# Kernel tuning notes

Measured on AMD Instinct MI355X. Metric: run time of the kernel, lower is better.

## Reference

```python
import jax, jax.numpy as jnp
import numpy as np

GROUP = 64   # quantization group size (nunchaku W4A4 default)
QMAX = 7.0   # symmetric int4 positive range


def setup_inputs() -> dict:
    key = jax.random.key(0)
    ks = jax.random.split(key, 6)
    T, K, N, R = 256, 3072, 3072, 32
    x = jax.random.normal(ks[0], (T, K), dtype=jnp.float32)
    # int4 weight codes stored as 0..15 (dequant subtracts zero-point 8)
    qweight = jax.random.randint(ks[1], (N, K), 0, 16, dtype=jnp.int32)
    # per-(out_channel, input_group) weight scales, small positive
    wscales = jax.random.uniform(ks[2], (N, K // GROUP), dtype=jnp.float32) * 0.02 + 1e-3
    lora_down = jax.random.normal(ks[3], (R, K), dtype=jnp.float32) / np.sqrt(K)
    lora_up = jax.random.normal(ks[4], (N, R), dtype=jnp.float32) / np.sqrt(R)
    bias = jax.random.normal(ks[5], (N,), dtype=jnp.float32) * 0.01
    return {"x": x, "qweight": qweight, "wscales": wscales,
            "lora_down": lora_down, "lora_up": lora_up, "bias": bias}


def _quantize_act(x):
    # per-token, per-group symmetric int4 fake-quant (quantize -> dequantize)
    T, K = x.shape
    xg = x.reshape(T, K // GROUP, GROUP)
    scale = jnp.maximum(jnp.max(jnp.abs(xg), axis=-1, keepdims=True) / QMAX, 1e-8)
    q = jnp.clip(jnp.round(xg / scale), -8.0, QMAX)
    return (q * scale).reshape(T, K)


def reference(x, qweight, wscales, lora_down, lora_up, bias):
    # Dequantize int4 weights: (code - 8) * per-group scale  -> [N, K]
    N, K = qweight.shape
    w = (qweight.astype(jnp.float32) - 8.0).reshape(N, K // GROUP, GROUP)
    w = (w * wscales[:, :, None]).reshape(N, K)
    # W4A4 main path: int4-quantized activations x dequantized int4 weights
    x_dq = _quantize_act(x)
    main = x_dq @ w.T                               # [T, N]
    # fused low-rank (SVDQuant LoRA) branch on full-precision activations
    lora = (x @ lora_down.T) @ lora_up.T            # [T, R] @ [R, N]
    return main + lora + bias
```

## Files before the change

kernel.cpp:

```cpp
#include <hip/hip_runtime.h>
#include <stdint.h>

#define T_DIM 256
#define K_DIM 3072
#define N_DIM 3072
#define R_DIM 32
#define KG    48
#define NSPLIT 6

#define PQ_BLOCKS 4608
#define QA_BLOCKS 3072
#define LM_BLOCKS 96

typedef __bf16 bf16x8 __attribute__((ext_vector_type(8)));
typedef float  f32x4  __attribute__((ext_vector_type(4)));
typedef unsigned short u16x8 __attribute__((ext_vector_type(8)));

__device__ __forceinline__ unsigned short f2bf(float f) {
    unsigned u = __builtin_bit_cast(unsigned, f);
    unsigned rounding = 0x7FFFu + ((u >> 16) & 1u);
    return (unsigned short)((u + rounding) >> 16);
}

__device__ __forceinline__ bf16x8 cvt8(const float* p) {
    float4 lo = ((const float4*)p)[0], hi = ((const float4*)p)[1];
    bf16x8 v;
    v[0] = (__bf16)lo.x; v[1] = (__bf16)lo.y; v[2] = (__bf16)lo.z; v[3] = (__bf16)lo.w;
    v[4] = (__bf16)hi.x; v[5] = (__bf16)hi.y; v[6] = (__bf16)hi.z; v[7] = (__bf16)hi.w;
    return v;
}

__global__ __launch_bounds__(256) void prep(
        const int*   __restrict__ qweight,
        const float* __restrict__ x,
        const float* __restrict__ lora_down,
        unsigned*       __restrict__ Qp,
        unsigned short* __restrict__ Ap,
        float*          __restrict__ Lm) {
    int blk = blockIdx.x;
    if (blk < PQ_BLOCKS) {
        size_t o = (size_t)blk * 256 + threadIdx.x;
        unsigned kt  = (unsigned)(o / 24576u);
        unsigned rem = (unsigned)(o % 24576u);
        unsigned n = rem >> 3, wi = rem & 7;
        const int4* p = (const int4*)(qweight + (size_t)n * K_DIM + (size_t)kt * 64 + wi * 8);
        int4 a = p[0], b = p[1];
        unsigned w = (unsigned)(a.x & 15)        | ((unsigned)(a.y & 15) << 4)
                   | ((unsigned)(a.z & 15) << 8) | ((unsigned)(a.w & 15) << 12)
                   | ((unsigned)(b.x & 15) << 16)| ((unsigned)(b.y & 15) << 20)
                   | ((unsigned)(b.z & 15) << 24)| ((unsigned)(b.w & 15) << 28);
        Qp[o] = w;
    } else if (blk < PQ_BLOCKS + QA_BLOCKS) {
        int widx = (blk - PQ_BLOCKS) * 4 + (threadIdx.x >> 6);
        int lane = threadIdx.x & 63;
        int t = widx / KG, g = widx % KG;
        float v = x[(size_t)t * K_DIM + g * 64 + lane];
        float a = fabsf(v);
        #pragma unroll
        for (int off = 32; off; off >>= 1) a = fmaxf(a, __shfl_xor(a, off));
        float scale = fmaxf(a / 7.0f, 1e-8f);
        float q = rintf(v / scale);
        q = fminf(fmaxf(q, -8.f), 7.f);
        Ap[(((size_t)g * 8 + (lane >> 3)) * 256 + t) * 8 + (lane & 7)] = f2bf(q * scale);
    } else {
        int kb = blk - PQ_BLOCKS - QA_BLOCKS;
        int lane = threadIdx.x & 63, wv = threadIdx.x >> 6;
        int mrow = lane & 15, quad = lane >> 4;
        int k0 = kb * 32 + quad * 8;
        bf16x8 a[4], b[2];
        #pragma unroll
        for (int mt = 0; mt < 4; ++mt)
            a[mt] = cvt8(x + (size_t)(wv * 64 + mt * 16 + mrow) * K_DIM + k0);
        #pragma unroll
        for (int nt = 0; nt < 2; ++nt)
            b[nt] = cvt8(lora_down + (size_t)(nt * 16 + mrow) * K_DIM + k0);
        f32x4 acc[4][2];
        f32x4 zero = {0.f, 0.f, 0.f, 0.f};
        #pragma unroll
        for (int i = 0; i < 4; ++i) { acc[i][0] = zero; acc[i][1] = zero; }
        #pragma unroll
        for (int mt = 0; mt < 4; ++mt)
            #pragma unroll
            for (int nt = 0; nt < 2; ++nt)
                acc[mt][nt] = __builtin_amdgcn_mfma_f32_16x16x32_bf16(
                    a[mt], b[nt], acc[mt][nt], 0, 0, 0);
        #pragma unroll
        for (int mt = 0; mt < 4; ++mt)
            #pragma unroll
            for (int nt = 0; nt < 2; ++nt)
                #pragma unroll
                for (int r = 0; r < 4; ++r)
                    atomicAdd(&Lm[(size_t)(wv * 64 + mt * 16 + quad * 4 + r) * R_DIM
                                  + nt * 16 + mrow], acc[mt][nt][r]);
    }
}

__global__ __launch_bounds__(256) void gemm_main(
        const uint4*    __restrict__ ApU,
        const unsigned* __restrict__ Qp,
        const float*    __restrict__ wscales,
        const float*    __restrict__ Lm,
        const float*    __restrict__ lora_up,
        float*          __restrict__ P) {
    __shared__ uint4 BsU[2][512];
    int nblk  = blockIdx.x;
    int mblk  = blockIdx.y;
    int split = blockIdx.z;
    int c0 = split * (KG / NSPLIT);
    int c1 = (split == NSPLIT - 1) ? KG + 1 : c0 + (KG / NSPLIT);
    int tid = threadIdx.x;
    int lane = tid & 63, wv = tid >> 6;
    int mrow = lane & 15, quad = lane >> 4;
    int n_row = tid >> 2, seg = tid & 3;
    const int nbase = nblk * 64;
    const int mbase = mblk * 128 + wv * 32;

    f32x4 acc[2][4];
    f32x4 zero = {0.f, 0.f, 0.f, 0.f};
    #pragma unroll
    for (int i = 0; i < 2; ++i)
        #pragma unroll
        for (int j = 0; j < 4; ++j) acc[i][j] = zero;

    uint2 ubc[2];
    float wsr[2];
    bf16x8 af[2][2][2];

    const float* wsrow = wscales + (size_t)(nbase + n_row) * KG;

    #define AFRAG(kt, ks, mt) \
        (*(const bf16x8*)&ApU[(size_t)(kt) * 2048 + ((ks) * 4 + quad) * 256 + \
                              mbase + (mt) * 16 + mrow])

    {
        #pragma unroll
        for (int ks = 0; ks < 2; ++ks)
            #pragma unroll
            for (int mt = 0; mt < 2; ++mt)
                af[0][ks][mt] = AFRAG(c0, ks, mt);
        const unsigned* q0 = Qp + ((size_t)c0 * N_DIM + nbase + n_row) * 8 + seg * 2;
        const unsigned* q1 = Qp + ((size_t)(c0 + 1) * N_DIM + nbase + n_row) * 8 + seg * 2;
        ubc[0] = *(const uint2*)q0;
        ubc[1] = *(const uint2*)q1;
        wsr[0] = wsrow[c0];
        wsr[1] = wsrow[c0 + 1];
    }

    #define STEP(PP, KT)                                                          \
    {                                                                             \
        constexpr int p = (PP);                                                   \
        const int kk = (KT);                                                      \
        if (kk < KG) {                                                            \
            float w = wsr[p];                                                     \
            float m8w = -8.0f * w;                                                \
            unsigned u0 = ubc[p].x, u1 = ubc[p].y;                                \
            unsigned e0 = u0 & 0x0F0F0F0Fu, od0 = (u0 >> 4) & 0x0F0F0F0Fu;        \
            unsigned e1 = u1 & 0x0F0F0F0Fu, od1 = (u1 >> 4) & 0x0F0F0F0Fu;        \
            bf16x8 v0, v1;                                                        \
            _Pragma("unroll")                                                     \
            for (int j = 0; j < 4; ++j) {                                         \
                v0[2*j]   = (__bf16)__builtin_fmaf((float)((e0  >> (8*j)) & 0xFFu), w, m8w); \
                v0[2*j+1] = (__bf16)__builtin_fmaf((float)((od0 >> (8*j)) & 0xFFu), w, m8w); \
                v1[2*j]   = (__bf16)__builtin_fmaf((float)((e1  >> (8*j)) & 0xFFu), w, m8w); \
                v1[2*j+1] = (__bf16)__builtin_fmaf((float)((od1 >> (8*j)) & 0xFFu), w, m8w); \
            }                                                                     \
            BsU[p][(seg * 2 + 0) * 64 + n_row] = __builtin_bit_cast(uint4, v0);   \
            BsU[p][(seg * 2 + 1) * 64 + n_row] = __builtin_bit_cast(uint4, v1);   \
        } else {                                                                  \
            bf16x8 v0 = __builtin_bit_cast(bf16x8, (u16x8)(0));                   \
            bf16x8 v1 = __builtin_bit_cast(bf16x8, (u16x8)(0));                   \
            if (seg < 2) {                                                        \
                const float* lu = lora_up + (size_t)(nbase + n_row) * R_DIM + seg * 16; \
                _Pragma("unroll")                                                 \
                for (int j = 0; j < 8; ++j) {                                     \
                    v0[j] = (__bf16)lu[j];                                        \
                    v1[j] = (__bf16)lu[8 + j];                                    \
                }                                                                 \
            }                                                                     \
            BsU[p][(seg * 2 + 0) * 64 + n_row] = __builtin_bit_cast(uint4, v0);   \
            BsU[p][(seg * 2 + 1) * 64 + n_row] = __builtin_bit_cast(uint4, v1);   \
        }                                                                         \
        __syncthreads();                                                          \
        if (kk + 2 < c1 && kk + 2 < KG) {                                         \
            const unsigned* q2 = Qp + ((size_t)(kk + 2) * N_DIM + nbase + n_row) * 8 + seg * 2; \
            ubc[p] = *(const uint2*)q2;                                           \
            wsr[p] = wsrow[kk + 2];                                               \
        }                                                                         \
        if (kk + 1 < c1) {                                                        \
            if (kk + 1 < KG) {                                                    \
                _Pragma("unroll")                                                 \
                for (int ks = 0; ks < 2; ++ks)                                    \
                    _Pragma("unroll")                                             \
                    for (int mt = 0; mt < 2; ++mt)                                \
                        af[p ^ 1][ks][mt] = AFRAG(kk + 1, ks, mt);                \
            } else {                                                              \
                _Pragma("unroll")                                                 \
                for (int mt = 0; mt < 2; ++mt) {                                  \
                    int row = mbase + mt * 16 + mrow;                             \
                    if (quad < 4)                                                 \
                        af[p ^ 1][0][mt] = cvt8(Lm + (size_t)row * R_DIM + quad * 8); \
                    else                                                          \
                        af[p ^ 1][0][mt] = __builtin_bit_cast(bf16x8, (u16x8)(0)); \
                    af[p ^ 1][1][mt] = __builtin_bit_cast(bf16x8, (u16x8)(0));    \
                }                                                                 \
            }                                                                     \
        }                                                                         \
        _Pragma("unroll")                                                         \
        for (int ks = 0; ks < 2; ++ks) {                                          \
            bf16x8 b[4];                                                          \
            _Pragma("unroll")                                                     \
            for (int nt = 0; nt < 4; ++nt)                                        \
                b[nt] = *(const bf16x8*)&BsU[p][(ks * 4 + quad) * 64 + nt * 16 + mrow]; \
            _Pragma("unroll")                                                     \
            for (int mt = 0; mt < 2; ++mt)                                        \
                _Pragma("unroll")                                                 \
                for (int nt = 0; nt < 4; ++nt)                                    \
                    acc[mt][nt] = __builtin_amdgcn_mfma_f32_16x16x32_bf16(        \
                        af[p][ks][mt], b[nt], acc[mt][nt], 0, 0, 0);              \
        }                                                                         \
    }

    int kt = c0;
    for (; kt + 1 < c1; kt += 2) {
        STEP(0, kt);
        STEP(1, kt + 1);
    }
    if (kt < c1) STEP(0, kt);

    #undef STEP
    #undef AFRAG
    float* Pp = P + (size_t)split * (T_DIM * N_DIM);
    #pragma unroll
    for (int nt = 0; nt < 4; ++nt) {
        int n = nbase + nt * 16 + mrow;
        #pragma unroll
        for (int mt = 0; mt < 2; ++mt) {
            int row0 = mblk * 128 + wv * 32 + mt * 16 + quad * 4;
            #pragma unroll
            for (int r = 0; r < 4; ++r)
                Pp[(size_t)(row0 + r) * N_DIM + n] = acc[mt][nt][r];
        }
    }
}

__global__ __launch_bounds__(256) void reduce_out(
        const float4* __restrict__ P, const float* __restrict__ bias,
        float4* __restrict__ out) {
    int i = blockIdx.x * 256 + threadIdx.x;
    const int STRIDE = T_DIM * N_DIM / 4;
    float4 bv = *(const float4*)&bias[(i * 4) % N_DIM];
    float4 o = bv;
    #pragma unroll
    for (int s = 0; s < NSPLIT; ++s) {
        float4 v = P[i + s * STRIDE];
        o.x += v.x; o.y += v.y; o.z += v.z; o.w += v.w;
    }
    out[i] = o;
}

extern "C" void kernel_launch(void* const* d_in, const int* in_sizes, int n_in,
                              void* d_out, int out_size, void* d_ws, size_t ws_size,
                              hipStream_t stream) {
    const float* x         = (const float*)d_in[0];
    const int*   qweight   = (const int*)d_in[1];
    const float* wscales   = (const float*)d_in[2];
    const float* lora_down = (const float*)d_in[3];
    const float* lora_up   = (const float*)d_in[4];
    const float* bias      = (const float*)d_in[5];

    char* wsp = (char*)d_ws;
    unsigned short* Ap = (unsigned short*)wsp;
    wsp += (size_t)KG * 2048 * 16;
    float* Lm = (float*)wsp;
    wsp += (size_t)T_DIM * R_DIM * 4;
    unsigned* Qp = (unsigned*)wsp;
    wsp += (size_t)N_DIM * (K_DIM / 8) * 4;
    float* P = (float*)wsp;

    hipMemsetAsync(Lm, 0, (size_t)T_DIM * R_DIM * sizeof(float), stream);
    prep<<<PQ_BLOCKS + QA_BLOCKS + LM_BLOCKS, 256, 0, stream>>>(
        qweight, x, lora_down, Qp, Ap, Lm);
    gemm_main<<<dim3(48, 2, NSPLIT), 256, 0, stream>>>(
        (const uint4*)Ap, Qp, wscales, Lm, lora_up, P);
    reduce_out<<<(T_DIM * N_DIM / 4) / 256, 256, 0, stream>>>(
        (const float4*)P, bias, (float4*)d_out);
}
```

Before: 117.4 us.

## Replace split-K partial buffer and reduce kernel with atomic accumulation into output

The prep kernel gains extra blocks that initialise the output with the broadcast bias. The GEMM then atomically adds each split-K partial tile straight into the output, so the per-split partial buffer and the separate reduce kernel go away. This removes one launch and the write and re-read of six full-size partial matrices. In exchange it adds global float atomics with six-way contention per element and makes the summation order nondeterministic. The LDS fragment load is also rewritten as a uint4 read plus bit_cast.

Measured after the change: 119.3 us. Within noise of the previous version (+1.6%).

```diff
diff --git a/kernel.cpp b/kernel.cpp
--- a/kernel.cpp
+++ b/kernel.cpp
@@ -11,6 +11,7 @@
 #define PQ_BLOCKS 4608
 #define QA_BLOCKS 3072
 #define LM_BLOCKS 96
+#define BO_BLOCKS 768
 
 typedef __bf16 bf16x8 __attribute__((ext_vector_type(8)));
 typedef float  f32x4  __attribute__((ext_vector_type(4)));
@@ -34,9 +35,11 @@
         const int*   __restrict__ qweight,
         const float* __restrict__ x,
         const float* __restrict__ lora_down,
+        const float* __restrict__ bias,
         unsigned*       __restrict__ Qp,
         unsigned short* __restrict__ Ap,
-        float*          __restrict__ Lm) {
+        float*          __restrict__ Lm,
+        float*          __restrict__ out) {
     int blk = blockIdx.x;
     if (blk < PQ_BLOCKS) {
         size_t o = (size_t)blk * 256 + threadIdx.x;
@@ -62,7 +65,7 @@
         float q = rintf(v / scale);
         q = fminf(fmaxf(q, -8.f), 7.f);
         Ap[(((size_t)g * 8 + (lane >> 3)) * 256 + t) * 8 + (lane & 7)] = f2bf(q * scale);
-    } else {
+    } else if (blk < PQ_BLOCKS + QA_BLOCKS + LM_BLOCKS) {
         int kb = blk - PQ_BLOCKS - QA_BLOCKS;
         int lane = threadIdx.x & 63, wv = threadIdx.x >> 6;
         int mrow = lane & 15, quad = lane >> 4;
@@ -92,6 +95,10 @@
                 for (int r = 0; r < 4; ++r)
                     atomicAdd(&Lm[(size_t)(wv * 64 + mt * 16 + quad * 4 + r) * R_DIM
                                   + nt * 16 + mrow], acc[mt][nt][r]);
+    } else {
+        int i = (blk - PQ_BLOCKS - QA_BLOCKS - LM_BLOCKS) * 256 + threadIdx.x;
+        float4 bv = *(const float4*)&bias[(i * 4) % N_DIM];
+        ((float4*)out)[i] = bv;
     }
 }
 
@@ -101,7 +108,7 @@
         const float*    __restrict__ wscales,
         const float*    __restrict__ Lm,
         const float*    __restrict__ lora_up,
-        float*          __restrict__ P) {
+        float*          __restrict__ out) {
     __shared__ uint4 BsU[2][512];
     int nblk  = blockIdx.x;
     int mblk  = blockIdx.y;
@@ -209,8 +216,10 @@
         for (int ks = 0; ks < 2; ++ks) {                                          \
             bf16x8 b[4];                                                          \
             _Pragma("unroll")                                                     \
-            for (int nt = 0; nt < 4; ++nt)                                        \
-                b[nt] = *(const bf16x8*)&BsU[p][(ks * 4 + quad) * 64 + nt * 16 + mrow]; \
+            for (int nt = 0; nt < 4; ++nt) {                                      \
+                uint4 tb = BsU[p][(ks * 4 + quad) * 64 + nt * 16 + mrow];         \
+                b[nt] = __builtin_bit_cast(bf16x8, tb);                           \
+            }                                                                     \
             _Pragma("unroll")                                                     \
             for (int mt = 0; mt < 2; ++mt)                                        \
                 _Pragma("unroll")                                                 \
@@ -229,7 +238,6 @@
 
     #undef STEP
     #undef AFRAG
-    float* Pp = P + (size_t)split * (T_DIM * N_DIM);
     #pragma unroll
     for (int nt = 0; nt < 4; ++nt) {
         int n = nbase + nt * 16 + mrow;
@@ -238,24 +246,9 @@
             int row0 = mblk * 128 + wv * 32 + mt * 16 + quad * 4;
             #pragma unroll
             for (int r = 0; r < 4; ++r)
-                Pp[(size_t)(row0 + r) * N_DIM + n] = acc[mt][nt][r];
+                atomicAdd(&out[(size_t)(row0 + r) * N_DIM + n], acc[mt][nt][r]);
         }
     }
-}
-
-__global__ __launch_bounds__(256) void reduce_out(
-        const float4* __restrict__ P, const float* __restrict__ bias,
-        float4* __restrict__ out) {
-    int i = blockIdx.x * 256 + threadIdx.x;
-    const int STRIDE = T_DIM * N_DIM / 4;
-    float4 bv = *(const float4*)&bias[(i * 4) % N_DIM];
-    float4 o = bv;
-    #pragma unroll
-    for (int s = 0; s < NSPLIT; ++s) {
-        float4 v = P[i + s * STRIDE];
-        o.x += v.x; o.y += v.y; o.z += v.z; o.w += v.w;
-    }
-    out[i] = o;
 }
 
 extern "C" void kernel_launch(void* const* d_in, const int* in_sizes, int n_in,
@@ -274,14 +267,10 @@
     float* Lm = (float*)wsp;
     wsp += (size_t)T_DIM * R_DIM * 4;
     unsigned* Qp = (unsigned*)wsp;
-    wsp += (size_t)N_DIM * (K_DIM / 8) * 4;
-    float* P = (float*)wsp;
 
     hipMemsetAsync(Lm, 0, (size_t)T_DIM * R_DIM * sizeof(float), stream);
-    prep<<<PQ_BLOCKS + QA_BLOCKS + LM_BLOCKS, 256, 0, stream>>>(
-        qweight, x, lora_down, Qp, Ap, Lm);
+    prep<<<PQ_BLOCKS + QA_BLOCKS + LM_BLOCKS + BO_BLOCKS, 256, 0, stream>>>(
+        qweight, x, lora_down, bias, Qp, Ap, Lm, (float*)d_out);
     gemm_main<<<dim3(48, 2, NSPLIT), 256, 0, stream>>>(
-        (const uint4*)Ap, Qp, wscales, Lm, lora_up, P);
-    reduce_out<<<(T_DIM * N_DIM / 4) / 256, 256, 0, stream>>>(
-        (const float4*)P, bias, (float4*)d_out);
-}
+        (const uint4*)Ap, Qp, wscales, Lm, lora_up, (float*)d_out);
+}
```
